# Kernel tuning notes

Hardware: AMD Instinct MI355X
Metric: run time of the kernel (lower is better)

## Reference

```python
import jax, jax.numpy as jnp
import numpy as np
from jax import lax

NUM_SEGMENTS = 50
HIDDEN = 128
IN_CH = 64
LOGSIG_DIM = IN_CH + IN_CH * (IN_CH - 1) // 2 + IN_CH  # level1 + Levy area + startpoint


def setup_inputs() -> dict:
    key = jax.random.key(0)
    k0, k1, k2, k3, k4 = jax.random.split(key, 5)
    B, C, T, V = 16, IN_CH, 200, 25
    x = jax.random.normal(k0, (B, C, T, V), dtype=jnp.float32)
    s = 1.0 / np.sqrt(HIDDEN).astype(np.float32)
    W_ih = jax.random.uniform(k1, (4 * HIDDEN, LOGSIG_DIM), jnp.float32, -s, s)
    W_hh = jax.random.uniform(k2, (4 * HIDDEN, HIDDEN), jnp.float32, -s, s)
    b_ih = jax.random.uniform(k3, (4 * HIDDEN,), jnp.float32, -s, s)
    b_hh = jax.random.uniform(k4, (4 * HIDDEN,), jnp.float32, -s, s)
    return {"x": x, "W_ih": W_ih, "W_hh": W_hh, "b_ih": b_ih, "b_hh": b_hh}


def _segment_logsig(xn):
    # xn: (N, C, T). Split T into NUM_SEGMENTS chunks; level-2 log-signature per chunk.
    N, C, T = xn.shape
    L = T // NUM_SEGMENTS  # points per segment
    p = xn.transpose(0, 2, 1).reshape(N, NUM_SEGMENTS, L, C)  # path points
    start = p[:, :, 0]                                  # (N,S,C) segment startpoint
    inc = p[:, :, 1:] - p[:, :, :-1]                    # (N,S,L-1,C) increments
    dev = p[:, :, :-1] - start[:, :, None]              # (N,S,L-1,C) p_t - p_0
    # Level-2 iterated integrals (cross terms): S2_ij = sum_t dev_t,i * inc_t,j
    S2 = jnp.einsum('nsti,nstj->nsij', dev, inc)        # (N,S,C,C)
    A = 0.5 * (S2 - S2.transpose(0, 1, 3, 2))           # Levy area (antisymmetric part)
    iu, ju = jnp.triu_indices(C, k=1)
    levy = A[:, :, iu, ju]                              # (N,S,C(C-1)/2)
    lvl1 = p[:, :, -1] - start                          # (N,S,C) level-1 term
    return jnp.concatenate([lvl1, levy, start], axis=-1)  # (N,S,LOGSIG_DIM)


def _lstm(seq, W_ih, W_hh, b_ih, b_hh):
    # seq: (N, S, F). Single-layer unidirectional LSTM, torch gate order (i,f,g,o).
    N = seq.shape[0]
    x_proj = jnp.einsum('nsf,gf->nsg', seq, W_ih) + b_ih + b_hh  # (N,S,4H)

    def step(carry, xt):
        h, c = carry
        gates = xt + h @ W_hh.T
        i, f, g, o = jnp.split(gates, 4, axis=-1)
        c = jax.nn.sigmoid(f) * c + jax.nn.sigmoid(i) * jnp.tanh(g)
        h = jax.nn.sigmoid(o) * jnp.tanh(c)
        return (h, c), h

    h0 = jnp.zeros((N, HIDDEN), seq.dtype)
    c0 = jnp.zeros((N, HIDDEN), seq.dtype)
    _, hs = lax.scan(step, (h0, c0), x_proj.transpose(1, 0, 2))
    return hs.transpose(1, 0, 2)  # (N,S,H)


def reference(x, W_ih, W_hh, b_ih, b_hh):
    B, C, T, V = x.shape
    xn = x.transpose(0, 3, 1, 2).reshape(B * V, C, T)
    ls = _segment_logsig(xn)                      # (B*V, S, LOGSIG_DIM)
    h = _lstm(ls, W_ih, W_hh, b_ih, b_hh)          # (B*V, S, H)
    out = h.reshape(B, V, NUM_SEGMENTS, HIDDEN).transpose(0, 3, 2, 1)
    return out  # (B, H, S, V)
```

## Files before the change

kernel.cpp:

```cpp
#include <hip/hip_runtime.h>
#include <stdint.h>

#define NSEG 50
#define HID 128
#define KDIM 2144
#define KD2 2240
#define KD2B 4480
#define NROW 20000
#define NROW_PAD 20224
#define GATES 512
#define NSEQ 400
#define NGRP 528

typedef __attribute__((ext_vector_type(8))) _Float16 f16x8;
typedef __attribute__((ext_vector_type(4))) _Float16 f16x4;
typedef __attribute__((ext_vector_type(4))) float f32x4;
typedef __attribute__((ext_vector_type(4))) uint32_t u32x4;

#define GLB_SPACE __attribute__((address_space(1)))
#define LDS_SPACE __attribute__((address_space(3)))

__device__ __forceinline__ void g2lds16(const void* g, void* l) {
    __builtin_amdgcn_global_load_lds((const GLB_SPACE uint32_t*)g,
                                     (LDS_SPACE uint32_t*)l, 16, 0, 0);
}

__device__ __forceinline__ int goff528(int i) {
    int n = 63 - i;
    int q = n >> 2, t = n & 3;
    return NGRP - (q + 1) * (2 * q + t);
}
__device__ __forceinline__ int ifromg(int g) {
    int i = 63 - (int)sqrtf(8.0f * (float)(NGRP - g));
    if (i < 0) i = 0;
    if (i > 62) i = 62;
    while (i > 0 && goff528(i) > g) i--;
    while (goff528(i + 1) <= g) i++;
    return i;
}

#define UVP(c) ((((c) & 3) << 4) | ((c) >> 2))

__global__ __launch_bounds__(512) void feat_kernel(const float* __restrict__ x,
                                                   const float* __restrict__ Wih,
                                                   const float* __restrict__ Whh,
                                                   const float* __restrict__ bih,
                                                   const float* __restrict__ bhh,
                                                   _Float16* __restrict__ feat,
                                                   _Float16* __restrict__ wh,
                                                   _Float16* __restrict__ whh16,
                                                   float* __restrict__ bias) {
    int bid = blockIdx.x;
    int tid = threadIdx.x;

    __shared__ float pbuf[64 * 101];
    __shared__ __align__(16) float4 uv4[25 * 64];

    if (bid >= 800) {
        int* kmap = (int*)pbuf;
        for (int k = tid; k < KD2; k += 512) {
            int orig;
            if (k < 64) {
                orig = k;
            } else if (k < 64 + 4 * NGRP) {
                int g = (k - 64) >> 2, p = (k - 64) & 3;
                int i = ifromg(g);
                int j = i + 1 + 4 * (g - goff528(i)) + p;
                orig = (j < 64) ? (64 + 63 * i - (i * (i - 1)) / 2 + (j - i - 1)) : -1;
            } else {
                orig = 2080 + (k - (64 + 4 * NGRP));
            }
            kmap[k] = orig;
        }
        __syncthreads();
        const int nwih = 512 * KD2;
        const int nwhh = 512 * HID;
        const int total = nwih + nwhh + 512;
        for (int idx = (bid - 800) * 512 + tid; idx < total; idx += 64 * 512) {
            if (idx < nwih) {
                int row = idx / KD2;
                int k = idx - row * KD2;
                int orig = kmap[k];
                wh[idx] = (orig >= 0) ? (_Float16)Wih[row * KDIM + orig] : (_Float16)0.0f;
            } else if (idx < nwih + nwhh) {
                int q = idx - nwih;
                whh16[q] = (_Float16)Whh[q];
            } else {
                int g = idx - nwih - nwhh;
                bias[g] = bih[g] + bhh[g];
            }
        }
        return;
    }

    int b = bid / NSEG;
    int s = bid - b * NSEG;

    for (int i = tid; i < 6400; i += 512) {
        int c = i / 100;
        int r = i - c * 100;
        pbuf[c * 101 + r] = x[(((size_t)b * 64 + c) * 200 + 4 * s) * 25 + r];
    }
    __syncthreads();

    for (int i = tid; i < 1600; i += 512) {
        int v = i >> 6;
        int c = i & 63;
        float p0 = pbuf[c * 101 + v];
        float p1 = pbuf[c * 101 + 25 + v];
        float p2 = pbuf[c * 101 + 50 + v];
        float p3 = pbuf[c * 101 + 75 + v];
        uv4[v * 64 + UVP(c)] = make_float4(p1 - p0, p2 - p0, p2 - p1, p3 - p2);
        size_t m = ((size_t)(b * 25 + v)) * NSEG + s;
        feat[m * KD2 + c] = (_Float16)(p3 - p0);
        feat[m * KD2 + (64 + 4 * NGRP) + c] = (_Float16)p0;
    }
    __syncthreads();

    for (int idx = tid; idx < 4 * NGRP; idx += 512) {
        int vb = idx / NGRP;
        int g = idx - vb * NGRP;
        int i = ifromg(g);
        int t = g - goff528(i);
        int j0 = i + 1 + 4 * t;
        int k0 = 64 + 4 * g;
        float msk[4];
        int jc[4];
#pragma unroll
        for (int p = 0; p < 4; p++) {
            int j = j0 + p;
            msk[p] = (j < 64) ? 0.5f : 0.0f;
            jc[p] = (j < 64) ? UVP(j) : UVP(63);
        }
        int ip = UVP(i);
        int v0 = (vb == 0) ? 0 : 6 * vb + 1;
        int vn = (vb == 0) ? 7 : 6;
        for (int vv = 0; vv < vn; vv++) {
            int v = v0 + vv;
            const float4* rowv = &uv4[v * 64];
            float4 a = rowv[ip];
            f16x4 o;
#pragma unroll
            for (int p = 0; p < 4; p++) {
                float4 bb = rowv[jc[p]];
                float val = msk[p] * (a.x * bb.z - bb.x * a.z + a.y * bb.w - bb.y * a.w);
                o[p] = (_Float16)val;
            }
            size_t m = ((size_t)(b * 25 + v)) * NSEG + s;
            *(f16x4*)(feat + m * KD2 + k0) = o;
        }
    }
}

__global__ __launch_bounds__(512, 2) void gemm_kernel(const _Float16* __restrict__ feat,
                                                      const _Float16* __restrict__ wh,
                                                      const float* __restrict__ bias,
                                                      _Float16* __restrict__ xproj2) {
    int bid = blockIdx.x;
    int mt = bid >> 1;
    int nb = bid & 1;
    int m0 = mt * 256;
    int n0 = nb * 256;
    int tid = threadIdx.x;
    int wave = tid >> 6;
    int lane = tid & 63;
    int quad = lane >> 4;
    int l15 = lane & 15;
    int wm = (wave >> 1) * 64;
    int wn = (wave & 1) * 128;

    __shared__ __align__(16) char lds[4][32768];

    const f32x4 z4 = {0.f, 0.f, 0.f, 0.f};
    f32x4 acc[4][8];
    for (int i = 0; i < 4; i++)
        for (int j = 0; j < 8; j++) acc[i][j] = z4;

    const char* featB = (const char*)feat;
    const char* whB = (const char*)wh;

    int lr = lane >> 2;
    int csw = (((lane & 3) ^ ((lane >> 3) & 3)) << 4);
    const char* aU0 = featB + (size_t)(m0 + wave * 16 + lr) * KD2B + csw;
    const char* aU1 = featB + (size_t)(m0 + (wave + 8) * 16 + lr) * KD2B + csw;
    const char* bU0 = whB + (size_t)(n0 + wave * 16 + lr) * KD2B + csw;
    const char* bU1 = whB + (size_t)(n0 + (wave + 8) * 16 + lr) * KD2B + csw;
    int dA0 = wave * 1024;
    int dA1 = (wave + 8) * 1024;
    int dB0 = 16384 + wave * 1024;
    int dB1 = 16384 + (wave + 8) * 1024;

    int frsw = ((quad ^ ((l15 >> 1) & 3)) << 4);

#define STAGE_HALF(h_) do {                                   \
        char* Hb = lds[(h_) & 3];                             \
        size_t kb = (size_t)(h_) * 64;                        \
        g2lds16(aU0 + kb, Hb + dA0);                          \
        g2lds16(aU1 + kb, Hb + dA1);                          \
        g2lds16(bU0 + kb, Hb + dB0);                          \
        g2lds16(bU1 + kb, Hb + dB1);                          \
    } while (0)

#define GPHASE(h_, VM, DO_STAGE) do {                                         \
        if (DO_STAGE) STAGE_HALF((h_) + 3);                                   \
        asm volatile("s_waitcnt vmcnt(" #VM ")" ::: "memory");                \
        __builtin_amdgcn_s_barrier();                                         \
        asm volatile("" ::: "memory");                                        \
        const char* Hc = lds[(h_) & 3];                                       \
        f16x8 af[4], bf[8];                                                   \
        for (int tt = 0; tt < 4; tt++)                                        \
            af[tt] = *(const f16x8*)(Hc + (wm + tt * 16 + l15) * 64 + frsw);  \
        for (int tt = 0; tt < 8; tt++)                                        \
            bf[tt] = *(const f16x8*)(Hc + 16384 + (wn + tt * 16 + l15) * 64 + frsw); \
        __builtin_amdgcn_s_setprio(1);                                        \
        for (int mtl = 0; mtl < 4; mtl++)                                     \
            for (int ntl = 0; ntl < 8; ntl++)                                 \
                acc[mtl][ntl] = __builtin_amdgcn_mfma_f32_16x16x32_f16(af[mtl], bf[ntl], acc[mtl][ntl], 0, 0, 0); \
        __builtin_amdgcn_s_setprio(0);                                        \
        asm volatile("" ::: "memory");                                        \
        __builtin_amdgcn_s_barrier();                                         \
    } while (0)

    STAGE_HALF(0);
    STAGE_HALF(1);
    STAGE_HALF(2);

    for (int h = 0; h < 67; h++) GPHASE(h, 12, true);
    GPHASE(67, 8, false);
    GPHASE(68, 4, false);
    GPHASE(69, 0, false);

#undef GPHASE
#undef STAGE_HALF

    __syncthreads();

    _Float16* ep = (_Float16*)lds;
    for (int p = 0; p < 2; p++) {
        if ((wave >> 2) == p) {
            for (int ntl = 0; ntl < 8; ntl++) {
                int nl = wn + ntl * 16 + l15;
                float bv = bias[n0 + nl];
                for (int mtl = 0; mtl < 4; mtl++)
                    for (int r = 0; r < 4; r++) {
                        int relm = wm - p * 128 + mtl * 16 + quad * 4 + r;
                        ep[relm * 260 + nl] = (_Float16)(acc[mtl][ntl][r] + bv);
                    }
            }
        }
        __syncthreads();
        for (int it = 0; it < 8; it++) {
            int rowp = it * 16 + (tid >> 5);
            int m = m0 + p * 128 + rowp;
            if (m < NROW) {
                unsigned q = (unsigned)m / 50u;
                unsigned s = (unsigned)m - q * 50u;
                const char* src = (const char*)ep + rowp * 520 + (tid & 31) * 16;
                char* dst = (char*)xproj2 + ((size_t)s * NSEQ + q) * 1024 + (size_t)n0 * 2 + (tid & 31) * 16;
                *(u32x4*)dst = *(const u32x4*)src;
            }
        }
        __syncthreads();
    }
}

__global__ __launch_bounds__(512, 2) void lstm_kernel(const _Float16* __restrict__ xproj2,
                                                      const _Float16* __restrict__ whh,
                                                      _Float16* __restrict__ hseq) {
    int bid = blockIdx.x;
    int tid = threadIdx.x;
    int wave = tid >> 6;
    int lane = tid & 63;
    int quad = lane >> 4;
    int col = lane & 15;
    int hid = wave * 16 + col;

    __shared__ __align__(16) char xbuf[25 * 4 * 1040];
    __shared__ __align__(16) _Float16 hst[NSEG * 4 * HID];
    __shared__ __align__(16) _Float16 hbuf[2][4 * 144];

    f16x8 bfrag[4][4];
    for (int g = 0; g < 4; g++) {
        int n = g * 128 + hid;
        for (int kq = 0; kq < 4; kq++)
            bfrag[g][kq] = *(const f16x8*)(whh + (size_t)n * HID + kq * 32 + quad * 8);
    }
    for (int i = tid; i < 2 * 4 * 144; i += 512) ((_Float16*)hbuf)[i] = (_Float16)0.0f;
    float cst = 0.0f;

    const char* xsrc = (const char*)xproj2;
    for (int r = wave; r < 100; r += 8)
        g2lds16(xsrc + ((size_t)((r >> 2) * NSEQ + bid * 4 + (r & 3))) * 1024 + lane * 16,
                xbuf + r * 1040);
    __syncthreads();

    const f32x4 z4 = {0.f, 0.f, 0.f, 0.f};
    for (int half = 0; half < 2; half++) {
        for (int ss = 0; ss < 25; ss++) {
            int s = half * 25 + ss;
            int cur = s & 1;
            int nxt = cur ^ 1;

            f16x8 afrag[4];
            for (int kq = 0; kq < 4; kq++)
                afrag[kq] = *(const f16x8*)(&hbuf[cur][(col & 3) * 144 + kq * 32 + quad * 8]);

            float xp[4];
            for (int g = 0; g < 4; g++)
                xp[g] = (float)(*(const _Float16*)(xbuf + (ss * 4 + quad) * 1040 +
                               (g * 128 + hid) * 2));

            f32x4 acc[4];
            for (int g = 0; g < 4; g++) {
                acc[g] = z4;
                for (int kq = 0; kq < 4; kq++)
                    acc[g] = __builtin_amdgcn_mfma_f32_16x16x32_f16(afrag[kq], bfrag[g][kq], acc[g], 0, 0, 0);
            }

            float gv[4];
            for (int g = 0; g < 4; g++) {
                float lo = (quad & 1) ? acc[g][1] : acc[g][0];
                float hi = (quad & 1) ? acc[g][3] : acc[g][2];
                gv[g] = (quad & 2) ? hi : lo;
            }

            float ip = gv[0] + xp[0];
            float fp = gv[1] + xp[1];
            float gp = gv[2] + xp[2];
            float op = gv[3] + xp[3];
            float si = __fdividef(1.0f, 1.0f + __expf(-ip));
            float sf = __fdividef(1.0f, 1.0f + __expf(-fp));
            float so = __fdividef(1.0f, 1.0f + __expf(-op));
            float eg = __expf(-2.0f * gp);
            float tg = __fdividef(1.0f - eg, 1.0f + eg);
            cst = sf * cst + si * tg;
            float ec = __expf(-2.0f * cst);
            float tc = __fdividef(1.0f - ec, 1.0f + ec);
            float hv = so * tc;
            _Float16 hv16 = (_Float16)hv;
            hbuf[nxt][quad * 144 + hid] = hv16;
            hst[(s * 4 + quad) * 128 + hid] = hv16;
            __syncthreads();
        }
        if (half == 0) {
            for (int r = wave; r < 100; r += 8)
                g2lds16(xsrc + ((size_t)((25 + (r >> 2)) * NSEQ + bid * 4 + (r & 3))) * 1024 + lane * 16,
                        xbuf + r * 1040);
            __syncthreads();
        }
    }

    const u32x4* src = (const u32x4*)hst;
    for (int i = tid; i < 3200; i += 512) {
        int s = i >> 6;
        int rem = i & 63;
        int seq = rem >> 4;
        int seg = rem & 15;
        u32x4 v = src[i];
        *(u32x4*)((char*)hseq + ((size_t)(s * NSEQ + bid * 4 + seq)) * 256 + seg * 16) = v;
    }
}

__global__ __launch_bounds__(256) void tr_kernel(const _Float16* __restrict__ hseq,
                                                 float* __restrict__ out) {
    int bid = blockIdx.x;
    int b = bid / NSEG;
    int s = bid - b * NSEG;
    int tid = threadIdx.x;

    __shared__ _Float16 buf[25 * 130];

    const uint32_t* src32 = (const uint32_t*)(hseq + ((size_t)s * NSEQ + b * 25) * HID);
    uint32_t* buf32 = (uint32_t*)buf;
    for (int i = tid; i < 1600; i += 256) {
        int v = i >> 6;
        int d = i & 63;
        buf32[v * 65 + d] = src32[i];
    }
    __syncthreads();
    for (int i = tid; i < 3200; i += 256) {
        int hid = i / 25;
        int v = i - hid * 25;
        out[(((size_t)b * 128 + hid) * NSEG + s) * 25 + v] = (float)buf[v * 130 + hid];
    }
}

extern "C" void kernel_launch(void* const* d_in, const int* in_sizes, int n_in,
                              void* d_out, int out_size, void* d_ws, size_t ws_size,
                              hipStream_t stream) {
    const float* x = (const float*)d_in[0];
    const float* Wih = (const float*)d_in[1];
    const float* Whh = (const float*)d_in[2];
    const float* bih = (const float*)d_in[3];
    const float* bhh = (const float*)d_in[4];
    float* out = (float*)d_out;

    char* ws = (char*)d_ws;
    size_t off = 0;
    _Float16* feat = (_Float16*)(ws + off);   off += (size_t)NROW_PAD * KD2 * 2;
    _Float16* xproj2 = (_Float16*)(ws + off); off += (size_t)NSEG * NSEQ * GATES * 2;
    _Float16* hseq = (_Float16*)(ws + off);   off += (size_t)NSEG * NSEQ * HID * 2;
    _Float16* wh = (_Float16*)(ws + off);     off += (size_t)512 * KD2 * 2;
    _Float16* whh16 = (_Float16*)(ws + off);  off += (size_t)512 * HID * 2;
    float* bias = (float*)(ws + off);         off += 512 * 4;

    hipLaunchKernelGGL(feat_kernel, dim3(864), dim3(512), 0, stream,
                       x, Wih, Whh, bih, bhh, feat, wh, whh16, bias);
    hipLaunchKernelGGL(gemm_kernel, dim3(158), dim3(512), 0, stream, feat, wh, bias, xproj2);
    hipLaunchKernelGGL(lstm_kernel, dim3(100), dim3(512), 0, stream, xproj2, whh16, hseq);
    hipLaunchKernelGGL(tr_kernel, dim3(16 * NSEG), dim3(256), 0, stream, hseq, out);
}
```

Before: 225.0 us.

## Retile input-projection GEMM into single-wave 80x128 blocks with XCD-aware mapping

The GEMM changes from 158 blocks of 512 threads with 256x256 tiles to 1000 single-wave blocks, each computing an 80x128 tile. This removes M padding and lets blocks cover all 256 CUs evenly. Block indices are remapped so neighbouring tiles land on the same XCD, and the pipeline becomes double-buffered with no barriers. The trade-off is much less operand reuse per tile, so more global and L2 traffic, and each wave has to hide its own load latency.

```diff
diff --git a/kernel.cpp b/kernel.cpp
--- a/kernel.cpp
+++ b/kernel.cpp
@@ -7,7 +7,7 @@
 #define KD2 2240
 #define KD2B 4480
 #define NROW 20000
-#define NROW_PAD 20224
+#define NROW_PAD 20000
 #define GATES 512
 #define NSEQ 400
 #define NGRP 528
@@ -152,115 +152,99 @@
     }
 }
 
-__global__ __launch_bounds__(512, 2) void gemm_kernel(const _Float16* __restrict__ feat,
-                                                      const _Float16* __restrict__ wh,
-                                                      const float* __restrict__ bias,
-                                                      _Float16* __restrict__ xproj2) {
+__global__ __launch_bounds__(64, 1) void gemm_kernel(const _Float16* __restrict__ feat,
+                                                     const _Float16* __restrict__ wh,
+                                                     const float* __restrict__ bias,
+                                                     _Float16* __restrict__ xproj2) {
     int bid = blockIdx.x;
-    int mt = bid >> 1;
-    int nb = bid & 1;
-    int m0 = mt * 256;
-    int n0 = nb * 256;
-    int tid = threadIdx.x;
-    int wave = tid >> 6;
-    int lane = tid & 63;
+    int xcd = bid & 7;
+    int idx = bid >> 3;
+    int wg = xcd * 125 + idx;
+    int mt = wg >> 2;
+    int nb = wg & 3;
+    int m0 = mt * 80;
+    int n0 = nb * 128;
+    int lane = threadIdx.x;
     int quad = lane >> 4;
     int l15 = lane & 15;
-    int wm = (wave >> 1) * 64;
-    int wn = (wave & 1) * 128;
-
-    __shared__ __align__(16) char lds[4][32768];
+
+    __shared__ __align__(16) char lds[2][13312];
 
     const f32x4 z4 = {0.f, 0.f, 0.f, 0.f};
-    f32x4 acc[4][8];
-    for (int i = 0; i < 4; i++)
+    f32x4 acc[5][8];
+#pragma unroll
+    for (int i = 0; i < 5; i++)
+#pragma unroll
         for (int j = 0; j < 8; j++) acc[i][j] = z4;
 
-    const char* featB = (const char*)feat;
-    const char* whB = (const char*)wh;
-
     int lr = lane >> 2;
-    int csw = (((lane & 3) ^ ((lane >> 3) & 3)) << 4);
-    const char* aU0 = featB + (size_t)(m0 + wave * 16 + lr) * KD2B + csw;
-    const char* aU1 = featB + (size_t)(m0 + (wave + 8) * 16 + lr) * KD2B + csw;
-    const char* bU0 = whB + (size_t)(n0 + wave * 16 + lr) * KD2B + csw;
-    const char* bU1 = whB + (size_t)(n0 + (wave + 8) * 16 + lr) * KD2B + csw;
-    int dA0 = wave * 1024;
-    int dA1 = (wave + 8) * 1024;
-    int dB0 = 16384 + wave * 1024;
-    int dB1 = 16384 + (wave + 8) * 1024;
-
-    int frsw = ((quad ^ ((l15 >> 1) & 3)) << 4);
-
-#define STAGE_HALF(h_) do {                                   \
-        char* Hb = lds[(h_) & 3];                             \
-        size_t kb = (size_t)(h_) * 64;                        \
-        g2lds16(aU0 + kb, Hb + dA0);                          \
-        g2lds16(aU1 + kb, Hb + dA1);                          \
-        g2lds16(bU0 + kb, Hb + dB0);                          \
-        g2lds16(bU1 + kb, Hb + dB1);                          \
+    int lc = (lane & 3) * 16;
+    const char* aS[5];
+    const char* bS[8];
+#pragma unroll
+    for (int u = 0; u < 5; u++)
+        aS[u] = (const char*)feat + (size_t)(m0 + u * 16 + lr) * KD2B + lc;
+#pragma unroll
+    for (int u = 0; u < 8; u++)
+        bS[u] = (const char*)wh + (size_t)(n0 + u * 16 + lr) * KD2B + lc;
+
+#define STAGE(h_) do {                                                        \
+        char* Hb = lds[(h_) & 1];                                             \
+        size_t kb = (size_t)(h_) * 64;                                        \
+        for (int u = 0; u < 5; u++) g2lds16(aS[u] + kb, Hb + u * 1024);       \
+        for (int u = 0; u < 8; u++) g2lds16(bS[u] + kb, Hb + 5120 + u * 1024);\
     } while (0)
 
-#define GPHASE(h_, VM, DO_STAGE) do {                                         \
-        if (DO_STAGE) STAGE_HALF((h_) + 3);                                   \
-        asm volatile("s_waitcnt vmcnt(" #VM ")" ::: "memory");                \
-        __builtin_amdgcn_s_barrier();                                         \
-        asm volatile("" ::: "memory");                                        \
-        const char* Hc = lds[(h_) & 3];                                       \
-        f16x8 af[4], bf[8];                                                   \
-        for (int tt = 0; tt < 4; tt++)                                        \
-            af[tt] = *(const f16x8*)(Hc + (wm + tt * 16 + l15) * 64 + frsw);  \
+#define GPHASE(h_, VMLIT, DO_STAGE) do {                                      \
+        asm volatile("s_waitcnt vmcnt(" #VMLIT ")" ::: "memory");             \
+        const char* Hc = lds[(h_) & 1];                                       \
+        f16x8 af[5], bf[8];                                                   \
+        for (int tt = 0; tt < 5; tt++)                                        \
+            af[tt] = *(const f16x8*)(Hc + (tt * 16 + l15) * 64 + quad * 16);  \
         for (int tt = 0; tt < 8; tt++)                                        \
-            bf[tt] = *(const f16x8*)(Hc + 16384 + (wn + tt * 16 + l15) * 64 + frsw); \
-        __builtin_amdgcn_s_setprio(1);                                        \
-        for (int mtl = 0; mtl < 4; mtl++)                                     \
+            bf[tt] = *(const f16x8*)(Hc + 5120 + (tt * 16 + l15) * 64 + quad * 16); \
+        asm volatile("s_waitcnt lgkmcnt(0)" ::: "memory");                    \
+        __builtin_amdgcn_sched_barrier(0);                                    \
+        if (DO_STAGE) STAGE((h_) + 2);                                        \
+        for (int mtl = 0; mtl < 5; mtl++)                                     \
             for (int ntl = 0; ntl < 8; ntl++)                                 \
                 acc[mtl][ntl] = __builtin_amdgcn_mfma_f32_16x16x32_f16(af[mtl], bf[ntl], acc[mtl][ntl], 0, 0, 0); \
-        __builtin_amdgcn_s_setprio(0);                                        \
-        asm volatile("" ::: "memory");                                        \
-        __builtin_amdgcn_s_barrier();                                         \
     } while (0)
 
-    STAGE_HALF(0);
-    STAGE_HALF(1);
-    STAGE_HALF(2);
-
-    for (int h = 0; h < 67; h++) GPHASE(h, 12, true);
-    GPHASE(67, 8, false);
-    GPHASE(68, 4, false);
+    STAGE(0);
+    STAGE(1);
+
+    for (int h = 0; h < 68; h++) GPHASE(h, 13, true);
+    GPHASE(68, 13, false);
     GPHASE(69, 0, false);
 
 #undef GPHASE
-#undef STAGE_HALF
-
-    __syncthreads();
+#undef STAGE
+
+    float bv[8];
+#pragma unroll
+    for (int ntl = 0; ntl < 8; ntl++) bv[ntl] = bias[n0 + ntl * 16 + l15];
 
     _Float16* ep = (_Float16*)lds;
-    for (int p = 0; p < 2; p++) {
-        if ((wave >> 2) == p) {
-            for (int ntl = 0; ntl < 8; ntl++) {
-                int nl = wn + ntl * 16 + l15;
-                float bv = bias[n0 + nl];
-                for (int mtl = 0; mtl < 4; mtl++)
-                    for (int r = 0; r < 4; r++) {
-                        int relm = wm - p * 128 + mtl * 16 + quad * 4 + r;
-                        ep[relm * 260 + nl] = (_Float16)(acc[mtl][ntl][r] + bv);
-                    }
-            }
-        }
-        __syncthreads();
-        for (int it = 0; it < 8; it++) {
-            int rowp = it * 16 + (tid >> 5);
-            int m = m0 + p * 128 + rowp;
-            if (m < NROW) {
-                unsigned q = (unsigned)m / 50u;
-                unsigned s = (unsigned)m - q * 50u;
-                const char* src = (const char*)ep + rowp * 520 + (tid & 31) * 16;
-                char* dst = (char*)xproj2 + ((size_t)s * NSEQ + q) * 1024 + (size_t)n0 * 2 + (tid & 31) * 16;
-                *(u32x4*)dst = *(const u32x4*)src;
-            }
-        }
-        __syncthreads();
+    for (int p = 0; p < 5; p++) {
+#pragma unroll
+        for (int ntl = 0; ntl < 8; ntl++)
+#pragma unroll
+            for (int r = 0; r < 4; r++)
+                ep[(quad * 4 + r) * 132 + ntl * 16 + l15] =
+                    (_Float16)(acc[p][ntl][r] + bv[ntl]);
+        asm volatile("s_waitcnt lgkmcnt(0)" ::: "memory");
+#pragma unroll
+        for (int t = 0; t < 4; t++) {
+            int rr = t * 4 + quad;
+            int m = m0 + p * 16 + rr;
+            unsigned q = (unsigned)m / 50u;
+            unsigned s = (unsigned)m - q * 50u;
+            const char* src = (const char*)ep + rr * 264 + l15 * 16;
+            char* dst = (char*)xproj2 + ((size_t)s * NSEQ + q) * 1024 + (size_t)n0 * 2 + l15 * 16;
+            *(u32x4*)dst = *(const u32x4*)src;
+        }
+        asm volatile("s_waitcnt lgkmcnt(0)" ::: "memory");
     }
 }
 
@@ -406,7 +390,7 @@
 
     hipLaunchKernelGGL(feat_kernel, dim3(864), dim3(512), 0, stream,
                        x, Wih, Whh, bih, bhh, feat, wh, whh16, bias);
-    hipLaunchKernelGGL(gemm_kernel, dim3(158), dim3(512), 0, stream, feat, wh, bias, xproj2);
+    hipLaunchKernelGGL(gemm_kernel, dim3(1000), dim3(64), 0, stream, feat, wh, bias, xproj2);
     hipLaunchKernelGGL(lstm_kernel, dim3(100), dim3(512), 0, stream, xproj2, whh16, hseq);
     hipLaunchKernelGGL(tr_kernel, dim3(16 * NSEG), dim3(256), 0, stream, hseq, out);
 }
```

After: 213.1 us. 5.3% less time.
